# Performance work log

Hardware: AMD Instinct MI355X
Metric: run time of the kernel (lower is better)

## Reference

```python
import jax, jax.numpy as jnp
import numpy as np
import math

# dims
B, DM, H, W = 8, 256, 32, 32
R = 4                      # num_rotations
DI = 2 * DM                # d_inner = expand * d_model = 512
DH = DI // 2               # 256
N = 16                     # d_state
K = 4                      # d_conv
DTR = math.ceil(DM / 16)   # dt_rank = 16


def _dwconv1d(x, w, b):
    # x: (B, C, L); w: (C, 1, K); torch padding='same' (even kernel: extra pad on right)
    lo = (K - 1) // 2
    y = jax.lax.conv_general_dilated(x, w, (1,), [(lo, K - 1 - lo)],
                                     dimension_numbers=('NCH', 'OIH', 'NCH'),
                                     feature_group_count=x.shape[1])
    return y + b[None, :, None]


def _conv2d(x, w, b=None, pad=0):
    y = jax.lax.conv_general_dilated(x, w, (1, 1), [(pad, pad), (pad, pad)],
                                     dimension_numbers=('NCHW', 'OIHW', 'NCHW'))
    return y if b is None else y + b[None, :, None, None]


def _selective_scan(u, delta, A, Bm, Cm):
    # u, delta: (b,r,d,l); A: (r,d,n); Bm, Cm: (b,r,n,l)
    xs = (jnp.moveaxis(delta, -1, 0), jnp.moveaxis(u, -1, 0),
          jnp.moveaxis(Bm, -1, 0), jnp.moveaxis(Cm, -1, 0))
    h0 = jnp.zeros(u.shape[:3] + (A.shape[-1],), u.dtype)  # (b,r,d,n)
    def step(h, inp):
        dt, ut, bt, ct = inp
        h = jnp.exp(dt[..., None] * A) * h + (dt * ut)[..., None] * bt[:, :, None, :]
        return h, jnp.einsum('brdn,brn->brd', h, ct)
    _, ys = jax.lax.scan(step, h0, xs)
    return jnp.moveaxis(ys, 0, -1)  # (b,r,d,l)


def setup_inputs() -> dict:
    key = jax.random.key(0)
    ks = iter(jax.random.split(key, 32))
    def rn(shape, s=0.02):
        return jax.random.normal(next(ks), shape, jnp.float32) * s
    return {
        'x': jax.random.normal(next(ks), (B, DM, H, W), jnp.float32),
        'in_proj_w': rn((DI, DM)),
        'out_proj_w': rn((DM, DI)),
        'conv_x_w': rn((R * DH, 1, K), 0.1), 'conv_x_b': rn((R * DH,), 0.1),
        'conv_z_w': rn((R * DH, 1, K), 0.1), 'conv_z_b': rn((R * DH,), 0.1),
        'x_proj_weight': rn((R, DTR + 2 * N, DH)),
        'dt_projs_weight': jax.random.uniform(next(ks), (R, DH, DTR)) * 0.1,
        'dt_projs_bias': jax.random.uniform(next(ks), (R, DH)) * 0.1,
        'A_logs': jax.random.normal(next(ks), (R * DH, N)) * 0.5,
        'Ds': jnp.ones((R * DH,), jnp.float32),
        'sa_w1': rn((DI // 4, R * DI, 3, 3)), 'sa_b1': jnp.zeros((DI // 4,)),
        'sa_w2': rn((R, DI // 4, 1, 1)), 'sa_b2': jnp.zeros((R,)),
        'ca_w1': rn((DI // 16, R * DI, 1, 1)),
        'ca_w2': rn((R, DI // 16, 1, 1)),
        'gate_w': rn((DI, 2 * DI, 1, 1)), 'gate_b': jnp.zeros((DI,)),
    }


def reference(x, in_proj_w, out_proj_w, conv_x_w, conv_x_b, conv_z_w, conv_z_b,
              x_proj_weight, dt_projs_weight, dt_projs_bias, A_logs, Ds,
              sa_w1, sa_b1, sa_w2, sa_b2, ca_w1, ca_w2, gate_w, gate_b):
    b = x.shape[0]
    L = H * W
    # in_proj (1x1 conv), then 4 rotations (first='l')
    xz = jnp.einsum('bchw,dc->bdhw', x, in_proj_w)                      # (b,DI,H,W)
    xz_rot = jnp.stack([jnp.rot90(xz, r, axes=(2, 3)) for r in range(R)], axis=1)
    xh, zh = jnp.split(xz_rot, 2, axis=2)                               # (b,R,DH,H,W)
    x_seq = jax.nn.silu(_dwconv1d(xh.reshape(b, R * DH, L), conv_x_w, conv_x_b))
    z_seq = jax.nn.silu(_dwconv1d(zh.reshape(b, R * DH, L), conv_z_w, conv_z_b))
    x4 = x_seq.reshape(b, R, DH, L)
    # input-dependent SSM params
    x_dbl = jnp.einsum('brdl,rkd->brkl', x4, x_proj_weight)
    dts, Bm, Cm = jnp.split(x_dbl, [DTR, DTR + N], axis=2)
    delta = jnp.einsum('brkl,rdk->brdl', dts, dt_projs_weight)
    delta = jax.nn.softplus(delta + dt_projs_bias[None, :, :, None])
    A = -jnp.exp(A_logs).reshape(R, DH, N)
    y = _selective_scan(x4, delta, A, Bm, Cm)
    y = y + Ds.reshape(R, DH)[None, :, :, None] * x4
    # MambaVision-style: concat scan output with gated z branch -> d_inner
    y = jnp.concatenate([y, z_seq.reshape(b, R, DH, L)], axis=2).reshape(b, R, DI, H, W)
    # undo rotations so branches are spatially aligned
    y = jnp.stack([jnp.rot90(y[:, r], -r, axes=(2, 3)) for r in range(R)], axis=1)
    # hybrid RotationAwareFusion
    y_flat = y.reshape(b, R * DI, H, W)
    sw = jax.nn.relu(_conv2d(y_flat, sa_w1, sa_b1, pad=1))
    sw = jax.nn.softmax(_conv2d(sw, sa_w2, sa_b2), axis=1)              # (b,R,H,W)
    spatial = jnp.einsum('brchw,brhw->bchw', y, sw)
    cavg = y.mean(axis=(3, 4)).reshape(b, R * DI, 1, 1)
    cw = jax.nn.relu(_conv2d(cavg, ca_w1))
    cw = jax.nn.softmax(_conv2d(cw, ca_w2), axis=1)[:, :, 0, 0]         # (b,R)
    channel = jnp.einsum('brchw,br->bchw', y, cw)
    g = jax.nn.sigmoid(_conv2d(jnp.concatenate([spatial, channel], axis=1), gate_w, gate_b))
    fused = g * spatial + (1.0 - g) * channel                           # (b,DI,H,W)
    out = jnp.einsum('bdhw,cd->bchw', fused, out_proj_w)
    return jax.nn.gelu(out)
```

## Files before the change

kernel.cpp:

```cpp
#include <hip/hip_runtime.h>
#include <math.h>


typedef _Float16 half8 __attribute__((ext_vector_type(8)));
typedef float f4 __attribute__((ext_vector_type(4)));

__device__ __forceinline__ int srcmap(int r, int l) {
  int i = l >> 5, j = l & 31;
  int h, w;
  if (r == 0)      { h = i;      w = j;      }
  else if (r == 1) { h = j;      w = 31 - i; }
  else if (r == 2) { h = 31 - i; w = 31 - j; }
  else             { h = 31 - j; w = i;      }
  return (h << 5) + w;
}

__device__ __forceinline__ float siluf(float x)    { return x / (1.f + __expf(-x)); }
__device__ __forceinline__ float sigmoidf_(float x){ return 1.f / (1.f + __expf(-x)); }
__device__ __forceinline__ float geluf(float x) {
  float x3 = x * x * x;
  return 0.5f * x * (1.f + tanhf(0.7978845608028654f * (x + 0.044715f * x3)));
}

__global__ void k_prep(const float* __restrict__ inw, const float* __restrict__ gw,
                       const float* __restrict__ opw,
                       float* __restrict__ inWT, _Float16* __restrict__ gwH,
                       _Float16* __restrict__ opH) {
  int idx = blockIdx.x * 256 + threadIdx.x;
  if (idx < 131072) {
    int c = idx >> 9, d = idx & 511;
    inWT[idx] = inw[d * 256 + c];
  } else if (idx < 655360) {
    int i = idx - 131072;
    gwH[i] = (_Float16)gw[i];
  } else {
    int i = idx - 655360;
    opH[i] = (_Float16)opw[i];
  }
}

__global__ void k_wprep(const float* __restrict__ saw1, _Float16* __restrict__ Whg2) {
  int o = blockIdx.x * 256 + threadIdx.x;
  int ci = o & 2047;
  int co = (o >> 11) & 127;
  int tap = o >> 18;
  size_t dst = (((size_t)(tap * 64 + (ci >> 5)) * 128) + co) * 32 + (ci & 31);
  Whg2[dst] = (_Float16)saw1[((size_t)co * 2048 + ci) * 9 + tap];
}

__global__ void __launch_bounds__(512) k_inproj(const float* __restrict__ x,
                                                const float* __restrict__ inWT,
                                                float* __restrict__ xz) {
  int d = threadIdx.x;
  int b = blockIdx.y;
  int p0 = blockIdx.x * 16;
  const float* xb = x + (size_t)(b * 256) * 1024 + p0;
  float acc[16];
#pragma unroll
  for (int j = 0; j < 16; ++j) acc[j] = 0.f;
  for (int c = 0; c < 256; ++c) {
    float w = inWT[c * 512 + d];
    const float* xr = xb + c * 1024;
#pragma unroll
    for (int q = 0; q < 4; ++q) {
      float4 v = *(const float4*)(xr + q * 4);
      acc[q*4+0] = fmaf(w, v.x, acc[q*4+0]);
      acc[q*4+1] = fmaf(w, v.y, acc[q*4+1]);
      acc[q*4+2] = fmaf(w, v.z, acc[q*4+2]);
      acc[q*4+3] = fmaf(w, v.w, acc[q*4+3]);
    }
  }
  float* o = xz + (size_t)(b * 512 + d) * 1024 + p0;
#pragma unroll
  for (int q = 0; q < 4; ++q) {
    float4 ov = {acc[q*4+0], acc[q*4+1], acc[q*4+2], acc[q*4+3]};
    *(float4*)(o + q * 4) = ov;
  }
}

__global__ void k_convx(const float* __restrict__ xz, const float* __restrict__ cw,
                        const float* __restrict__ cb, float* __restrict__ xseq) {
  int l  = blockIdx.x * 256 + threadIdx.x;
  int rd = blockIdx.y; int r = rd >> 8; int d = rd & 255;
  int b  = blockIdx.z;
  float w0 = cw[rd*4+0], w1 = cw[rd*4+1], w2 = cw[rd*4+2], w3 = cw[rd*4+3];
  float acc = cb[rd];
  const float* src = xz + (size_t)(b * 512 + d) * 1024;
  if (l - 1 >= 0)   acc = fmaf(w0, src[srcmap(r, l - 1)], acc);
  acc = fmaf(w1, src[srcmap(r, l)], acc);
  if (l + 1 < 1024) acc = fmaf(w2, src[srcmap(r, l + 1)], acc);
  if (l + 2 < 1024) acc = fmaf(w3, src[srcmap(r, l + 2)], acc);
  xseq[((size_t)(b * 4 + r) * 256 + d) * 1024 + l] = siluf(acc);
}

__global__ void k_convz(const float* __restrict__ xz, const float* __restrict__ cw,
                        const float* __restrict__ cb, float* __restrict__ Y) {
  int l  = blockIdx.x * 256 + threadIdx.x;
  int rd = blockIdx.y; int r = rd >> 8; int d = rd & 255;
  int b  = blockIdx.z;
  float w0 = cw[rd*4+0], w1 = cw[rd*4+1], w2 = cw[rd*4+2], w3 = cw[rd*4+3];
  float acc = cb[rd];
  const float* src = xz + (size_t)(b * 512 + 256 + d) * 1024;
  if (l - 1 >= 0)   acc = fmaf(w0, src[srcmap(r, l - 1)], acc);
  acc = fmaf(w1, src[srcmap(r, l)], acc);
  if (l + 1 < 1024) acc = fmaf(w2, src[srcmap(r, l + 1)], acc);
  if (l + 2 < 1024) acc = fmaf(w3, src[srcmap(r, l + 2)], acc);
  Y[((size_t)(b * 4 + r) * 512 + 256 + d) * 1024 + l] = siluf(acc);
}

__global__ void __launch_bounds__(256) k_xdblT(const float* __restrict__ xseq,
                                               const float* __restrict__ xpw,
                                               float* __restrict__ xdT) {
  int ch = blockIdx.x;
  int br = blockIdx.y;
  int r  = br & 3;
  int c  = threadIdx.x & 31;
  int kq = threadIdx.x >> 5;
  const float* xs = xseq + (size_t)(br * 256) * 1024 + ch * 32 + c;
  const float* w  = xpw + (r * 48 + kq * 6) * 256;
  float acc[6] = {0.f, 0.f, 0.f, 0.f, 0.f, 0.f};
  for (int d = 0; d < 256; ++d) {
    float xv = xs[(size_t)d * 1024];
#pragma unroll
    for (int j = 0; j < 6; ++j) acc[j] = fmaf(w[j * 256 + d], xv, acc[j]);
  }
  float* o = xdT + ((size_t)(br * 32 + ch) * 32 + c) * 48 + kq * 6;
#pragma unroll
  for (int j = 0; j < 6; ++j) o[j] = acc[j];
}

__global__ void __launch_bounds__(256) k_scanA(
    const float* __restrict__ xseq, const float* __restrict__ xdT,
    const float* __restrict__ dtw_, const float* __restrict__ dtb_,
    const float* __restrict__ alogs,
    float* __restrict__ aprodg, float* __restrict__ Yc) {
  int ch = blockIdx.x;
  int br = blockIdx.y; int r = br & 3;
  int d  = threadIdx.x;
  int rd = r * 256 + d;
  f4 w0 = *(const f4*)&dtw_[rd * 16], w1 = *(const f4*)&dtw_[rd * 16 + 4],
     w2 = *(const f4*)&dtw_[rd * 16 + 8], w3 = *(const f4*)&dtw_[rd * 16 + 12];
  float A2[16], h[16], ap[16];
#pragma unroll
  for (int n = 0; n < 16; ++n) A2[n] = -__expf(alogs[rd * 16 + n]) * 1.44269504f;
#pragma unroll
  for (int n = 0; n < 16; ++n) { h[n] = 0.f; ap[n] = 1.f; }
  float bias = dtb_[rd];
  __shared__ __align__(16) float t2[1536];
  const float* xd = xdT + (size_t)(br * 32 + ch) * 1536;
  for (int i = threadIdx.x; i < 384; i += 256) ((f4*)t2)[i] = ((const f4*)xd)[i];
  __syncthreads();
  const float* us = xseq + (size_t)(br * 256 + d) * 1024 + ch * 32;
  for (int c4 = 0; c4 < 8; ++c4) {
    float4 uv = *(const float4*)(us + c4 * 4);
    float uarr[4] = {uv.x, uv.y, uv.z, uv.w};
#pragma unroll
    for (int cc = 0; cc < 4; ++cc) {
      const f4* row = (const f4*)&t2[(c4 * 4 + cc) * 48];
      f4 td0 = row[0], td1 = row[1], td2 = row[2], td3 = row[3];
      float delta = bias
        + td0[0]*w0[0] + td0[1]*w0[1] + td0[2]*w0[2] + td0[3]*w0[3]
        + td1[0]*w1[0] + td1[1]*w1[1] + td1[2]*w1[2] + td1[3]*w1[3]
        + td2[0]*w2[0] + td2[1]*w2[1] + td2[2]*w2[2] + td2[3]*w2[3]
        + td3[0]*w3[0] + td3[1]*w3[1] + td3[2]*w3[2] + td3[3]*w3[3];
      float sp = (delta > 20.f) ? delta : __logf(1.f + __expf(delta));
      float du = sp * uarr[cc];
      f4 tb[4] = {row[4], row[5], row[6], row[7]};
#pragma unroll
      for (int n = 0; n < 16; ++n) {
        float e = exp2f(sp * A2[n]);
        h[n] = fmaf(e, h[n], du * tb[n >> 2][n & 3]);
        ap[n] *= e;
      }
    }
  }
  float* apo = aprodg + ((size_t)(br * 32 + ch) * 256 + d) * 16;
  float* hco = Yc + (size_t)(br * 512 + d) * 1024 + ch * 32;
#pragma unroll
  for (int n = 0; n < 16; ++n) { apo[n] = ap[n]; hco[n] = h[n]; }
}

__global__ void k_scanB(const float* __restrict__ aprodg, float* __restrict__ Yc) {
  int t  = blockIdx.x * 256 + threadIdx.x;
  int br = t >> 12;
  int dn = t & 4095;
  int d = dn >> 4, n = dn & 15;
  float h = 0.f;
  for (int c = 0; c < 32; ++c) {
    size_t ao = (size_t)(br * 32 + c) * 4096 + dn;
    size_t yo = (size_t)(br * 512 + d) * 1024 + c * 32 + n;
    float hin = h;
    h = fmaf(aprodg[ao], h, Yc[yo]);
    Yc[yo] = hin;
  }
}

__global__ void __launch_bounds__(256) k_scanC(
    const float* __restrict__ xseq, const float* __restrict__ xdT,
    const float* __restrict__ dtw_, const float* __restrict__ dtb_,
    const float* __restrict__ alogs, const float* __restrict__ ds_,
    float* __restrict__ Y) {
  int ch = blockIdx.x;
  int br = blockIdx.y; int r = br & 3;
  int d  = threadIdx.x;
  int rd = r * 256 + d;
  f4 w0 = *(const f4*)&dtw_[rd * 16], w1 = *(const f4*)&dtw_[rd * 16 + 4],
     w2 = *(const f4*)&dtw_[rd * 16 + 8], w3 = *(const f4*)&dtw_[rd * 16 + 12];
  float A2[16], h[16];
#pragma unroll
  for (int n = 0; n < 16; ++n) A2[n] = -__expf(alogs[rd * 16 + n]) * 1.44269504f;
  float bias = dtb_[rd];
  float dsv  = ds_[rd];
  __shared__ __align__(16) float t2[1536];
  __shared__ float yt[32][257];
  const float* xd = xdT + (size_t)(br * 32 + ch) * 1536;
  for (int i = threadIdx.x; i < 384; i += 256) ((f4*)t2)[i] = ((const f4*)xd)[i];
  float* ybase = Y + (size_t)(br * 512 + d) * 1024 + ch * 32;
#pragma unroll
  for (int n = 0; n < 16; ++n) h[n] = ybase[n];
  __syncthreads();
  const float* us = xseq + (size_t)(br * 256 + d) * 1024 + ch * 32;
  for (int c4 = 0; c4 < 8; ++c4) {
    float4 uv = *(const float4*)(us + c4 * 4);
    float uarr[4] = {uv.x, uv.y, uv.z, uv.w};
#pragma unroll
    for (int cc = 0; cc < 4; ++cc) {
      int c = c4 * 4 + cc;
      const f4* row = (const f4*)&t2[c * 48];
      f4 td0 = row[0], td1 = row[1], td2 = row[2], td3 = row[3];
      float delta = bias
        + td0[0]*w0[0] + td0[1]*w0[1] + td0[2]*w0[2] + td0[3]*w0[3]
        + td1[0]*w1[0] + td1[1]*w1[1] + td1[2]*w1[2] + td1[3]*w1[3]
        + td2[0]*w2[0] + td2[1]*w2[1] + td2[2]*w2[2] + td2[3]*w2[3]
        + td3[0]*w3[0] + td3[1]*w3[1] + td3[2]*w3[2] + td3[3]*w3[3];
      float sp = (delta > 20.f) ? delta : __logf(1.f + __expf(delta));
      float du = sp * uarr[cc];
      f4 tb[4] = {row[4], row[5], row[6], row[7]};
      f4 tc[4] = {row[8], row[9], row[10], row[11]};
      float acc = 0.f;
#pragma unroll
      for (int n = 0; n < 16; ++n) {
        float e = exp2f(sp * A2[n]);
        h[n] = fmaf(e, h[n], du * tb[n >> 2][n & 3]);
        acc  = fmaf(h[n], tc[n >> 2][n & 3], acc);
      }
      yt[c][d] = fmaf(dsv, uarr[cc], acc);
    }
  }
  __syncthreads();
  for (int i = threadIdx.x; i < 2048; i += 256) {
    int dd = i >> 3, lq = i & 7;
    f4 v = {yt[lq * 4 + 0][dd], yt[lq * 4 + 1][dd], yt[lq * 4 + 2][dd], yt[lq * 4 + 3][dd]};
    *(f4*)(Y + (size_t)(br * 512 + dd) * 1024 + ch * 32 + lq * 4) = v;
  }
}

__global__ void k_ytr(const float* __restrict__ Y, _Float16* __restrict__ Ytg) {
  __shared__ float t[32][132];
  int l0  = blockIdx.x * 128;
  int ci0 = blockIdx.y * 32;
  int b   = blockIdx.z;
  int r   = ci0 >> 9;
  const float* src = Y + ((size_t)(b * 2048 + ci0)) * 1024 + l0;
#pragma unroll
  for (int i = 0; i < 16; ++i) {
    int idx = threadIdx.x + i * 256;
    int ci = idx >> 7, pp = idx & 127;
    t[ci][pp] = src[(size_t)ci * 1024 + pp];
  }
  __syncthreads();
  int pp = threadIdx.x >> 1;
  int ch = (threadIdx.x & 1) * 16;
  _Float16 buf[16];
#pragma unroll
  for (int j = 0; j < 16; ++j) buf[j] = (_Float16)t[ch + j][pp];
  int pix = srcmap(r, l0 + pp);
  _Float16* dst = Ytg + ((size_t)(b * 1024) + pix) * 2048 + ci0 + ch;
  *(float4*)dst = *(const float4*)buf;
  *(float4*)(dst + 8) = *(const float4*)(buf + 8);
}

__global__ void __launch_bounds__(256, 2) k_samfma(const _Float16* __restrict__ Ytg,
                                                   const _Float16* __restrict__ Whg2,
                                                   float* __restrict__ cpart) {
  __shared__ __align__(16) _Float16 As[6][32][40];
  __shared__ __align__(16) _Float16 Bs[9][64][40];
  int L = blockIdx.x;
  int ks = L & 7;
  int rem = L >> 3;
  int b = rem >> 3, rg = rem & 7;
  int tid = threadIdx.x;
  int wid = tid >> 6, lane = tid & 63;
  int r = lane & 15, g = lane >> 4;
  const _Float16* Yb = Ytg + (size_t)b * (1024 * 2048);
  const half8 zero8 = {0, 0, 0, 0, 0, 0, 0, 0};

  int srow[3], scol[3], sci8[3], srcoff[3]; bool sok[3];
#pragma unroll
  for (int i = 0; i < 3; ++i) {
    int unit = tid + i * 256;
    srow[i] = unit >> 7; scol[i] = (unit >> 2) & 31; sci8[i] = unit & 3;
    int grow = rg * 4 - 1 + srow[i];
    sok[i] = ((unsigned)grow < 32u);
    srcoff[i] = ((sok[i] ? grow : 0) * 32 + scol[i]) * 2048 + sci8[i] * 8;
  }
  int bcol = tid >> 2, bci8 = tid & 3;
  int ci_base = ks * 256;

  for (int coh = 0; coh < 2; ++coh) {
    f4 acc[2][4];
#pragma unroll
    for (int mi = 0; mi < 2; ++mi)
#pragma unroll
      for (int ni = 0; ni < 4; ++ni) acc[mi][ni] = (f4){0.f, 0.f, 0.f, 0.f};

    half8 pa[3], pb[9];
#pragma unroll
    for (int i = 0; i < 3; ++i) {
      half8 v = *(const half8*)(Yb + srcoff[i] + ci_base);
      pa[i] = sok[i] ? v : zero8;
    }
#pragma unroll
    for (int j = 0; j < 9; ++j)
      pb[j] = *(const half8*)(Whg2 + (((size_t)(j * 64 + ks * 8) * 128) + coh * 64 + bcol) * 32 + bci8 * 8);

    for (int ch = 0; ch < 8; ++ch) {
      __syncthreads();
#pragma unroll
      for (int i = 0; i < 3; ++i)
        *(half8*)&As[srow[i]][scol[i]][sci8[i] * 8] = pa[i];
#pragma unroll
      for (int j = 0; j < 9; ++j)
        *(half8*)&Bs[j][bcol][bci8 * 8] = pb[j];
      if (ch < 7) {
        int ci0 = ci_base + (ch + 1) * 32;
#pragma unroll
        for (int i = 0; i < 3; ++i) {
          half8 v = *(const half8*)(Yb + srcoff[i] + ci0);
          pa[i] = sok[i] ? v : zero8;
        }
        int cic = ks * 8 + ch + 1;
#pragma unroll
        for (int j = 0; j < 9; ++j)
          pb[j] = *(const half8*)(Whg2 + (((size_t)(j * 64 + cic) * 128) + coh * 64 + bcol) * 32 + bci8 * 8);
      }
      __syncthreads();

#pragma unroll
      for (int tap = 0; tap < 9; ++tap) {
        const int dh = tap / 3 - 1, dw = tap % 3 - 1;
        int lrow = wid + dh + 1;
        half8 av[2], bv[4];
#pragma unroll
        for (int mi = 0; mi < 2; ++mi) {
          int lcol = mi * 16 + r + dw;
          bool ok = ((unsigned)lcol < 32u);
          half8 v = *(const half8*)&As[lrow][lcol & 31][g * 8];
          av[mi] = ok ? v : zero8;
        }
#pragma unroll
        for (int ni = 0; ni < 4; ++ni)
          bv[ni] = *(const half8*)&Bs[tap][ni * 16 + r][g * 8];
#pragma unroll
        for (int mi = 0; mi < 2; ++mi)
#pragma unroll
          for (int ni = 0; ni < 4; ++ni)
            acc[mi][ni] = __builtin_amdgcn_mfma_f32_16x16x32_f16(av[mi], bv[ni], acc[mi][ni], 0, 0, 0);
      }
    }

    float* cp = cpart + (size_t)ks * (8192 * 128);
    int basepix = b * 1024 + (rg * 4 + wid) * 32;
#pragma unroll
    for (int mi = 0; mi < 2; ++mi)
#pragma unroll
      for (int ni = 0; ni < 4; ++ni) {
        int co = coh * 64 + ni * 16 + r;
#pragma unroll
        for (int j = 0; j < 4; ++j)
          cp[(size_t)(basepix + mi * 16 + g * 4 + j) * 128 + co] = acc[mi][ni][j];
      }
    __syncthreads();
  }
}

__global__ void __launch_bounds__(256) k_saconv2f(const float* __restrict__ cpart,
                                                  const float* __restrict__ sab1,
                                                  const float* __restrict__ saw2,
                                                  const float* __restrict__ sab2,
                                                  float* __restrict__ swout) {
  int tid = threadIdx.x;
  int pixg = tid >> 3, cig = tid & 7;
  int p = blockIdx.x * 32 + pixg;
  int b = blockIdx.y;
  int pix = b * 1024 + p;
  const float* c0 = cpart + (size_t)pix * 128 + cig * 16;
  float a0 = 0.f, a1 = 0.f, a2 = 0.f, a3 = 0.f;
#pragma unroll
  for (int j4 = 0; j4 < 4; ++j4) {
    float sx = 0.f, sy = 0.f, sz = 0.f, sw_ = 0.f;
#pragma unroll
    for (int k = 0; k < 8; ++k) {
      float4 v = *(const float4*)(c0 + (size_t)k * 1048576 + j4 * 4);
      sx += v.x; sy += v.y; sz += v.z; sw_ += v.w;
    }
    int ci = cig * 16 + j4 * 4;
    float v0 = fmaxf(sx + sab1[ci],     0.f);
    float v1 = fmaxf(sy + sab1[ci + 1], 0.f);
    float v2 = fmaxf(sz + sab1[ci + 2], 0.f);
    float v3 = fmaxf(sw_ + sab1[ci + 3], 0.f);
    a0 = fmaf(v0, saw2[ci], fmaf(v1, saw2[ci+1], fmaf(v2, saw2[ci+2], fmaf(v3, saw2[ci+3], a0))));
    a1 = fmaf(v0, saw2[128+ci], fmaf(v1, saw2[128+ci+1], fmaf(v2, saw2[128+ci+2], fmaf(v3, saw2[128+ci+3], a1))));
    a2 = fmaf(v0, saw2[256+ci], fmaf(v1, saw2[256+ci+1], fmaf(v2, saw2[256+ci+2], fmaf(v3, saw2[256+ci+3], a2))));
    a3 = fmaf(v0, saw2[384+ci], fmaf(v1, saw2[384+ci+1], fmaf(v2, saw2[384+ci+2], fmaf(v3, saw2[384+ci+3], a3))));
  }
#pragma unroll
  for (int off = 4; off > 0; off >>= 1) {
    a0 += __shfl_down(a0, off, 8);
    a1 += __shfl_down(a1, off, 8);
    a2 += __shfl_down(a2, off, 8);
    a3 += __shfl_down(a3, off, 8);
  }
  if (cig == 0) {
    a0 += sab2[0]; a1 += sab2[1]; a2 += sab2[2]; a3 += sab2[3];
    float m = fmaxf(fmaxf(a0, a1), fmaxf(a2, a3));
    float e0 = __expf(a0 - m), e1 = __expf(a1 - m), e2 = __expf(a2 - m), e3 = __expf(a3 - m);
    float inv = 1.f / (e0 + e1 + e2 + e3);
    swout[(b * 4 + 0) * 1024 + p] = e0 * inv;
    swout[(b * 4 + 1) * 1024 + p] = e1 * inv;
    swout[(b * 4 + 2) * 1024 + p] = e2 * inv;
    swout[(b * 4 + 3) * 1024 + p] = e3 * inv;
  }
}

__global__ void k_cavg(const float* __restrict__ Y, float* __restrict__ cavg) {
  int gidq = blockIdx.x * 256 + threadIdx.x;
  int row = gidq >> 2, q = gidq & 3;
  const float4* yr = (const float4*)(Y + (size_t)row * 1024 + q * 256);
  float s = 0.f;
  for (int i = 0; i < 64; ++i) {
    float4 v = yr[i];
    s += v.x + v.y + v.z + v.w;
  }
  s += __shfl_down(s, 2, 4);
  s += __shfl_down(s, 1, 4);
  if (q == 0) cavg[row] = s * (1.f / 1024.f);
}

__global__ void k_cw(const float* __restrict__ cavg, const float* __restrict__ caw1,
                     const float* __restrict__ caw2, float* __restrict__ cwout) {
  int b = blockIdx.x;
  int t = threadIdx.x;
  __shared__ float hid[32];
  __shared__ float vv[4];
  if (t < 32) {
    float a = 0.f;
    const float* cv = cavg + b * 2048;
    const float* wr = caw1 + t * 2048;
    for (int i = 0; i < 2048; ++i) a = fmaf(wr[i], cv[i], a);
    hid[t] = fmaxf(a, 0.f);
  }
  __syncthreads();
  if (t < 4) {
    float a = 0.f;
    for (int i = 0; i < 32; ++i) a = fmaf(caw2[t * 32 + i], hid[i], a);
    vv[t] = a;
  }
  __syncthreads();
  if (t < 4) {
    float m = fmaxf(fmaxf(vv[0], vv[1]), fmaxf(vv[2], vv[3]));
    float e = __expf(vv[t] - m);
    float s = __expf(vv[0] - m) + __expf(vv[1] - m) + __expf(vv[2] - m) + __expf(vv[3] - m);
    cwout[b * 4 + t] = e / s;
  }
}

__global__ void __launch_bounds__(256) k_catH(const _Float16* __restrict__ Ytg,
                                              const float* __restrict__ swv,
                                              const float* __restrict__ cwv,
                                              _Float16* __restrict__ catO) {
  int p0 = blockIdx.x * 64, c0 = blockIdx.y * 64, b = blockIdx.z;
  int pp = threadIdx.x >> 2, cs = (threadIdx.x & 3) * 16;
  int pix = p0 + pp;
  const _Float16* src = Ytg + (size_t)(b * 1024 + pix) * 2048 + c0 + cs;
  float accS[16], accC[16];
#pragma unroll
  for (int j = 0; j < 16; ++j) { accS[j] = 0.f; accC[j] = 0.f; }
#pragma unroll
  for (int r = 0; r < 4; ++r) {
    half8 v0 = *(const half8*)(src + r * 512);
    half8 v1 = *(const half8*)(src + r * 512 + 8);
    float sw = swv[(size_t)(b * 4 + r) * 1024 + pix];
    float cw = cwv[b * 4 + r];
#pragma unroll
    for (int j = 0; j < 8; ++j) {
      float f0 = (float)v0[j], f1 = (float)v1[j];
      accS[j]     = fmaf(f0, sw, accS[j]);
      accS[j + 8] = fmaf(f1, sw, accS[j + 8]);
      accC[j]     = fmaf(f0, cw, accC[j]);
      accC[j + 8] = fmaf(f1, cw, accC[j + 8]);
    }
  }
  _Float16 os[16], oc[16];
#pragma unroll
  for (int j = 0; j < 16; ++j) { os[j] = (_Float16)accS[j]; oc[j] = (_Float16)accC[j]; }
  _Float16* dst = catO + ((size_t)(b * 1024) + pix) * 1024;
  *(half8*)(dst + c0 + cs)       = *(half8*)os;
  *(half8*)(dst + c0 + cs + 8)   = *(half8*)(os + 8);
  *(half8*)(dst + 512 + c0 + cs)     = *(half8*)oc;
  *(half8*)(dst + 512 + c0 + cs + 8) = *(half8*)(oc + 8);
}

__global__ void __launch_bounds__(256) k_gatemfma(const _Float16* __restrict__ catO,
                                                  const _Float16* __restrict__ gwH,
                                                  const float* __restrict__ gb,
                                                  _Float16* __restrict__ fusedH) {
  int wid = threadIdx.x >> 6, lane = threadIdx.x & 63;
  int r = lane & 15, g = lane >> 4;
  int p0 = blockIdx.x * 128 + (wid >> 1) * 64;
  int c0 = blockIdx.y * 128 + (wid & 1) * 64;
  int b  = blockIdx.z;
  const _Float16* Cb = catO + (size_t)b * (1024 * 1024);
  f4 acc[4][4];
#pragma unroll
  for (int mi = 0; mi < 4; ++mi)
#pragma unroll
    for (int ni = 0; ni < 4; ++ni) acc[mi][ni] = (f4){0.f, 0.f, 0.f, 0.f};
  for (int kk = 0; kk < 1024; kk += 32) {
    half8 av[4], bv[4];
#pragma unroll
    for (int mi = 0; mi < 4; ++mi)
      av[mi] = *(const half8*)(Cb + (size_t)(p0 + mi * 16 + r) * 1024 + kk + g * 8);
#pragma unroll
    for (int ni = 0; ni < 4; ++ni)
      bv[ni] = *(const half8*)(gwH + (size_t)(c0 + ni * 16 + r) * 1024 + kk + g * 8);
#pragma unroll
    for (int mi = 0; mi < 4; ++mi)
#pragma unroll
      for (int ni = 0; ni < 4; ++ni)
        acc[mi][ni] = __builtin_amdgcn_mfma_f32_16x16x32_f16(av[mi], bv[ni], acc[mi][ni], 0, 0, 0);
  }
#pragma unroll
  for (int ni = 0; ni < 4; ++ni) {
    int c = c0 + ni * 16 + r;
    float bias = gb[c];
#pragma unroll
    for (int mi = 0; mi < 4; ++mi)
#pragma unroll
      for (int j = 0; j < 4; ++j) {
        int pix = p0 + mi * 16 + g * 4 + j;
        const _Float16* rowp = Cb + (size_t)pix * 1024 + c;
        float sp = (float)rowp[0], ch = (float)rowp[512];
        float gt = sigmoidf_(acc[mi][ni][j] + bias);
        fusedH[((size_t)(b * 1024) + pix) * 512 + c] = (_Float16)(gt * sp + (1.f - gt) * ch);
      }
  }
}

__global__ void __launch_bounds__(256) k_outprojmfma(const _Float16* __restrict__ fusedH,
                                                     const _Float16* __restrict__ opH,
                                                     float* __restrict__ out) {
  int wid = threadIdx.x >> 6, lane = threadIdx.x & 63;
  int r = lane & 15, g = lane >> 4;
  int m0 = blockIdx.x * 64;
  int n0 = blockIdx.y * 256 + wid * 64;
  int b  = blockIdx.z;
  f4 acc[4][4];
#pragma unroll
  for (int mi = 0; mi < 4; ++mi)
#pragma unroll
    for (int ni = 0; ni < 4; ++ni) acc[mi][ni] = (f4){0.f, 0.f, 0.f, 0.f};
  for (int kk = 0; kk < 512; kk += 32) {
    half8 av[4], bv[4];
#pragma unroll
    for (int mi = 0; mi < 4; ++mi)
      av[mi] = *(const half8*)(opH + (size_t)(m0 + mi * 16 + r) * 512 + kk + g * 8);
#pragma unroll
    for (int ni = 0; ni < 4; ++ni)
      bv[ni] = *(const half8*)(fusedH + ((size_t)(b * 1024) + n0 + ni * 16 + r) * 512 + kk + g * 8);
#pragma unroll
    for (int mi = 0; mi < 4; ++mi)
#pragma unroll
      for (int ni = 0; ni < 4; ++ni)
        acc[mi][ni] = __builtin_amdgcn_mfma_f32_16x16x32_f16(av[mi], bv[ni], acc[mi][ni], 0, 0, 0);
  }
#pragma unroll
  for (int mi = 0; mi < 4; ++mi)
#pragma unroll
    for (int ni = 0; ni < 4; ++ni) {
      int pix = n0 + ni * 16 + r;
#pragma unroll
      for (int j = 0; j < 4; ++j) {
        int co = m0 + mi * 16 + g * 4 + j;
        out[((size_t)(b * 256) + co) * 1024 + pix] = geluf(acc[mi][ni][j]);
      }
    }
}

extern "C" void kernel_launch(void* const* d_in, const int* in_sizes, int n_in,
                              void* d_out, int out_size, void* d_ws, size_t ws_size,
                              hipStream_t stream) {
  const float* x    = (const float*)d_in[0];
  const float* inw  = (const float*)d_in[1];
  const float* opw  = (const float*)d_in[2];
  const float* cxw  = (const float*)d_in[3];
  const float* cxb  = (const float*)d_in[4];
  const float* czw  = (const float*)d_in[5];
  const float* czb  = (const float*)d_in[6];
  const float* xpw  = (const float*)d_in[7];
  const float* dtw  = (const float*)d_in[8];
  const float* dtb  = (const float*)d_in[9];
  const float* alog = (const float*)d_in[10];
  const float* ds   = (const float*)d_in[11];
  const float* saw1 = (const float*)d_in[12];
  const float* sab1 = (const float*)d_in[13];
  const float* saw2 = (const float*)d_in[14];
  const float* sab2 = (const float*)d_in[15];
  const float* caw1 = (const float*)d_in[16];
  const float* caw2 = (const float*)d_in[17];
  const float* gw   = (const float*)d_in[18];
  const float* gb   = (const float*)d_in[19];

  float* ws = (float*)d_ws;
  float* xz   = ws + 0;
  float* xseq = ws + 4194304;
  float* xdT  = ws + 12582912;
  float* Y    = ws + 14155776;
  float* swb  = ws + 31981568;
  float* cavg = ws + 32014336;
  float* cwb  = ws + 32030720;
  float* inWT = ws + 32030752;
  float* opHF = ws + 32161824;
  float* gwHF = ws + 32292896;
  float* WhgF = ws + 32817184;
  float* aprodg = xz;
  float* Cpart  = Y;
  _Float16* Ytg    = (_Float16*)xseq;
  _Float16* catO   = (_Float16*)xz;
  _Float16* fusedH = (_Float16*)xseq;
  _Float16* Whg2 = (_Float16*)WhgF;
  _Float16* gwH = (_Float16*)gwHF;
  _Float16* opH = (_Float16*)opHF;

  k_prep<<<3072, 256, 0, stream>>>(inw, gw, opw, inWT, gwH, opH);
  k_wprep<<<9216, 256, 0, stream>>>(saw1, Whg2);
  k_inproj<<<dim3(64, 8), 512, 0, stream>>>(x, inWT, xz);
  k_convx<<<dim3(4, 1024, 8), 256, 0, stream>>>(xz, cxw, cxb, xseq);
  k_convz<<<dim3(4, 1024, 8), 256, 0, stream>>>(xz, czw, czb, Y);
  k_xdblT<<<dim3(32, 32), 256, 0, stream>>>(xseq, xpw, xdT);
  k_scanA<<<dim3(32, 32), 256, 0, stream>>>(xseq, xdT, dtw, dtb, alog, aprodg, Y);
  k_scanB<<<512, 256, 0, stream>>>(aprodg, Y);
  k_scanC<<<dim3(32, 32), 256, 0, stream>>>(xseq, xdT, dtw, dtb, alog, ds, Y);
  k_ytr<<<dim3(8, 64, 8), 256, 0, stream>>>(Y, Ytg);
  k_cavg<<<256, 256, 0, stream>>>(Y, cavg);
  k_cw<<<8, 64, 0, stream>>>(cavg, caw1, caw2, cwb);
  k_samfma<<<512, 256, 0, stream>>>(Ytg, Whg2, Cpart);
  k_saconv2f<<<dim3(32, 8), 256, 0, stream>>>(Cpart, sab1, saw2, sab2, swb);
  k_catH<<<dim3(16, 8, 8), 256, 0, stream>>>(Ytg, swb, cwb, catO);
  k_gatemfma<<<dim3(8, 4, 8), 256, 0, stream>>>(catO, gwH, gb, fusedH);
  k_outprojmfma<<<dim3(4, 4, 8), 256, 0, stream>>>(fusedH, opH, (float*)d_out);
}
```

Baseline: 522.8 us.

## Fuse x/z depthwise convs with shared-memory staging and tile x_proj loads

Merges the two rotated depthwise conv kernels into one that loads each (b,d) row of x and z into shared memory once and produces all four rotations from it, with vectorized float4 stores. This replaces scattered rotated global gathers and removes a launch. The x_proj (xdblT) kernel now stages a 256x32 tile of xseq in padded shared memory and reads weights as float4, cutting strided global loads. The fused conv grid is much smaller (2048 blocks), which may reduce parallelism, and the rotated shared-memory reads can hit bank conflicts.

```diff
diff --git a/kernel.cpp b/kernel.cpp
--- a/kernel.cpp
+++ b/kernel.cpp
@@ -78,34 +78,53 @@
   }
 }
 
-__global__ void k_convx(const float* __restrict__ xz, const float* __restrict__ cw,
-                        const float* __restrict__ cb, float* __restrict__ xseq) {
-  int l  = blockIdx.x * 256 + threadIdx.x;
-  int rd = blockIdx.y; int r = rd >> 8; int d = rd & 255;
-  int b  = blockIdx.z;
-  float w0 = cw[rd*4+0], w1 = cw[rd*4+1], w2 = cw[rd*4+2], w3 = cw[rd*4+3];
-  float acc = cb[rd];
-  const float* src = xz + (size_t)(b * 512 + d) * 1024;
-  if (l - 1 >= 0)   acc = fmaf(w0, src[srcmap(r, l - 1)], acc);
-  acc = fmaf(w1, src[srcmap(r, l)], acc);
-  if (l + 1 < 1024) acc = fmaf(w2, src[srcmap(r, l + 1)], acc);
-  if (l + 2 < 1024) acc = fmaf(w3, src[srcmap(r, l + 2)], acc);
-  xseq[((size_t)(b * 4 + r) * 256 + d) * 1024 + l] = siluf(acc);
-}
-
-__global__ void k_convz(const float* __restrict__ xz, const float* __restrict__ cw,
-                        const float* __restrict__ cb, float* __restrict__ Y) {
-  int l  = blockIdx.x * 256 + threadIdx.x;
-  int rd = blockIdx.y; int r = rd >> 8; int d = rd & 255;
-  int b  = blockIdx.z;
-  float w0 = cw[rd*4+0], w1 = cw[rd*4+1], w2 = cw[rd*4+2], w3 = cw[rd*4+3];
-  float acc = cb[rd];
-  const float* src = xz + (size_t)(b * 512 + 256 + d) * 1024;
-  if (l - 1 >= 0)   acc = fmaf(w0, src[srcmap(r, l - 1)], acc);
-  acc = fmaf(w1, src[srcmap(r, l)], acc);
-  if (l + 1 < 1024) acc = fmaf(w2, src[srcmap(r, l + 1)], acc);
-  if (l + 2 < 1024) acc = fmaf(w3, src[srcmap(r, l + 2)], acc);
-  Y[((size_t)(b * 4 + r) * 512 + 256 + d) * 1024 + l] = siluf(acc);
+__global__ void __launch_bounds__(256) k_conv(const float* __restrict__ xz,
+                                              const float* __restrict__ cxw,
+                                              const float* __restrict__ cxb,
+                                              const float* __restrict__ czw,
+                                              const float* __restrict__ czb,
+                                              float* __restrict__ xseq,
+                                              float* __restrict__ Y) {
+  int d = blockIdx.x;
+  int b = blockIdx.y;
+  __shared__ float xs_t[1024];
+  __shared__ float zs_t[1024];
+  int t4 = threadIdx.x * 4;
+  *(float4*)&xs_t[t4] = *(const float4*)(xz + ((size_t)(b * 512 + d)) * 1024 + t4);
+  *(float4*)&zs_t[t4] = *(const float4*)(xz + ((size_t)(b * 512 + 256 + d)) * 1024 + t4);
+  __syncthreads();
+#pragma unroll
+  for (int r = 0; r < 4; ++r) {
+    int rd = r * 256 + d;
+    float xw0 = cxw[rd*4+0], xw1 = cxw[rd*4+1], xw2 = cxw[rd*4+2], xw3 = cxw[rd*4+3];
+    float zw0 = czw[rd*4+0], zw1 = czw[rd*4+1], zw2 = czw[rd*4+2], zw3 = czw[rd*4+3];
+    float xbi = cxb[rd], zbi = czb[rd];
+    float xo[4], zo[4];
+#pragma unroll
+    for (int q = 0; q < 4; ++q) {
+      int l = t4 + q;
+      float ax = xbi, az = zbi;
+      if (l - 1 >= 0) {
+        int s = srcmap(r, l - 1);
+        ax = fmaf(xw0, xs_t[s], ax); az = fmaf(zw0, zs_t[s], az);
+      }
+      {
+        int s = srcmap(r, l);
+        ax = fmaf(xw1, xs_t[s], ax); az = fmaf(zw1, zs_t[s], az);
+      }
+      if (l + 1 < 1024) {
+        int s = srcmap(r, l + 1);
+        ax = fmaf(xw2, xs_t[s], ax); az = fmaf(zw2, zs_t[s], az);
+      }
+      if (l + 2 < 1024) {
+        int s = srcmap(r, l + 2);
+        ax = fmaf(xw3, xs_t[s], ax); az = fmaf(zw3, zs_t[s], az);
+      }
+      xo[q] = siluf(ax); zo[q] = siluf(az);
+    }
+    *(float4*)(xseq + ((size_t)(b * 4 + r) * 256 + d) * 1024 + t4) = *(float4*)xo;
+    *(float4*)(Y + ((size_t)(b * 4 + r) * 512 + 256 + d) * 1024 + t4) = *(float4*)zo;
+  }
 }
 
 __global__ void __launch_bounds__(256) k_xdblT(const float* __restrict__ xseq,
@@ -114,15 +133,31 @@
   int ch = blockIdx.x;
   int br = blockIdx.y;
   int r  = br & 3;
+  __shared__ float xs_t[256][33];
+  const float* base = xseq + (size_t)(br * 256) * 1024 + ch * 32;
+  {
+    int c4 = threadIdx.x & 7;
+    int drow = threadIdx.x >> 3;
+#pragma unroll
+    for (int p = 0; p < 8; ++p) {
+      int dd = p * 32 + drow;
+      float4 v = *(const float4*)(base + (size_t)dd * 1024 + c4 * 4);
+      xs_t[dd][c4*4+0] = v.x; xs_t[dd][c4*4+1] = v.y;
+      xs_t[dd][c4*4+2] = v.z; xs_t[dd][c4*4+3] = v.w;
+    }
+  }
+  __syncthreads();
   int c  = threadIdx.x & 31;
   int kq = threadIdx.x >> 5;
-  const float* xs = xseq + (size_t)(br * 256) * 1024 + ch * 32 + c;
-  const float* w  = xpw + (r * 48 + kq * 6) * 256;
+  const float* w = xpw + (r * 48 + kq * 6) * 256;
   float acc[6] = {0.f, 0.f, 0.f, 0.f, 0.f, 0.f};
-  for (int d = 0; d < 256; ++d) {
-    float xv = xs[(size_t)d * 1024];
-#pragma unroll
-    for (int j = 0; j < 6; ++j) acc[j] = fmaf(w[j * 256 + d], xv, acc[j]);
+  for (int d0 = 0; d0 < 256; d0 += 4) {
+    float x0 = xs_t[d0][c], x1 = xs_t[d0+1][c], x2 = xs_t[d0+2][c], x3 = xs_t[d0+3][c];
+#pragma unroll
+    for (int j = 0; j < 6; ++j) {
+      float4 wv = *(const float4*)(w + j * 256 + d0);
+      acc[j] = fmaf(wv.x, x0, fmaf(wv.y, x1, fmaf(wv.z, x2, fmaf(wv.w, x3, acc[j]))));
+    }
   }
   float* o = xdT + ((size_t)(br * 32 + ch) * 32 + c) * 48 + kq * 6;
 #pragma unroll
@@ -645,8 +680,7 @@
   k_prep<<<3072, 256, 0, stream>>>(inw, gw, opw, inWT, gwH, opH);
   k_wprep<<<9216, 256, 0, stream>>>(saw1, Whg2);
   k_inproj<<<dim3(64, 8), 512, 0, stream>>>(x, inWT, xz);
-  k_convx<<<dim3(4, 1024, 8), 256, 0, stream>>>(xz, cxw, cxb, xseq);
-  k_convz<<<dim3(4, 1024, 8), 256, 0, stream>>>(xz, czw, czb, Y);
+  k_conv<<<dim3(256, 8), 256, 0, stream>>>(xz, cxw, cxb, czw, czb, xseq, Y);
   k_xdblT<<<dim3(32, 32), 256, 0, stream>>>(xseq, xpw, xdT);
   k_scanA<<<dim3(32, 32), 256, 0, stream>>>(xseq, xdT, dtw, dtb, alog, aprodg, Y);
   k_scanB<<<512, 256, 0, stream>>>(aprodg, Y);
```

New measurement: 454.2 us. 1.15x faster.
